# Kernel tuning notes

Measured on AMD Instinct MI355X. Metric: run time of the kernel, lower is better.

## Reference

```python
import jax, jax.numpy as jnp
import numpy as np

EMBED_DIM = 768
HIDDEN = 768


def setup_inputs() -> dict:
    key = jax.random.key(0)
    k1, k2, k3, k4 = jax.random.split(key, 4)
    doc_embed = jax.random.normal(k1, (32, 1024, EMBED_DIM), dtype=jnp.float32)
    query_embed = jax.random.normal(k2, (32, 128, EMBED_DIM), dtype=jnp.float32)
    # nn.Linear params: weight [H, E], bias [H]
    bound = 1.0 / np.sqrt(EMBED_DIM)
    W = jax.random.uniform(k3, (HIDDEN, EMBED_DIM), minval=-bound, maxval=bound, dtype=jnp.float32)
    b = jax.random.uniform(k4, (HIDDEN,), minval=-bound, maxval=bound, dtype=jnp.float32)
    return {"doc_embed": doc_embed, "query_embed": query_embed, "W": W, "b": b}


def reference(doc_embed, query_embed, W, b):
    # shared linear projection + ReLU
    doc_o = jax.nn.relu(jnp.einsum('bde,he->bdh', doc_embed, W) + b)    # [B, Ld, H]
    query_o = jax.nn.relu(jnp.einsum('bqe,he->bqh', query_embed, W) + b)  # [B, Lq, H]
    # unscaled cross-attention scores over query positions
    scores = jnp.einsum('bdh,bqh->bdq', doc_o, query_o)  # [B, Ld, Lq]
    attn = jax.nn.softmax(scores, axis=-1)
    out = jnp.einsum('bdq,bqe->bde', attn, query_embed)  # [B, Ld, E]
    return out
```

## Files before the change

### kernel.cpp

```cpp
#include <hip/hip_runtime.h>

typedef _Float16 f16x8 __attribute__((ext_vector_type(8)));
typedef float f32x4 __attribute__((ext_vector_type(4)));

#define EMB 768
#define LQ 128
#define LD 1024
#define NB 32

typedef const __attribute__((address_space(1))) char gas_char;
typedef __attribute__((address_space(3))) char las_char;

__device__ __forceinline__ void gload16(const void* g, void* l) {
    __builtin_amdgcn_global_load_lds((gas_char*)g, (las_char*)l, 16, 0, 0);
}

#define SWZ(row, ch) ((row) * 64 + ((((ch) ^ ((row) & 7))) * 8))

__device__ __forceinline__ void stage_tile(const _Float16* g, _Float16* l, int wave, int lane) {
#pragma unroll
    for (int i = 0; i < 4; ++i) {
        const int idx = i * 256 + wave * 64 + lane;
        const int row = idx >> 3, ch = idx & 7;
        const int lch = ch ^ (row & 7);
        gload16(g + (size_t)row * EMB + lch * 8, l + (size_t)(i * 256 + wave * 64) * 8);
    }
}

__global__ void cvt8_kernel(const float* __restrict__ in, _Float16* __restrict__ out, int n8) {
    int i = blockIdx.x * 256 + threadIdx.x;
    if (i >= n8) return;
    const float4 a = ((const float4*)in)[2 * i];
    const float4 b = ((const float4*)in)[2 * i + 1];
    f16x8 o;
    o[0] = (_Float16)a.x; o[1] = (_Float16)a.y; o[2] = (_Float16)a.z; o[3] = (_Float16)a.w;
    o[4] = (_Float16)b.x; o[5] = (_Float16)b.y; o[6] = (_Float16)b.z; o[7] = (_Float16)b.w;
    ((f16x8*)out)[i] = o;
}

__global__ void make_vt_kernel(const float* __restrict__ Q, _Float16* __restrict__ VT) {
    int i = blockIdx.x * 256 + threadIdx.x;
    if (i >= NB * EMB * LQ) return;
    int q = i % LQ;
    int e = (i / LQ) % EMB;
    int b = i / (LQ * EMB);
    VT[i] = (_Float16)Q[((size_t)b * LQ + q) * EMB + e];
}

__global__ __launch_bounds__(256) void proj128_kernel(
    const _Float16* __restrict__ A, const _Float16* __restrict__ B,
    const float* __restrict__ bias, _Float16* __restrict__ OUT) {
    __shared__ __align__(16) _Float16 smem[32768];
    const int tid = threadIdx.x, wave = tid >> 6, lane = tid & 63;
    const int wr = wave >> 1, wc = wave & 1;
    const int lr = lane & 15, lkg = lane >> 4;
    const int row0 = blockIdx.x * 128, col0 = blockIdx.y * 128;
    const _Float16* ga = A + (size_t)row0 * EMB;
    const _Float16* gb = B + (size_t)col0 * EMB;

    f32x4 acc[4][4];
#pragma unroll
    for (int m = 0; m < 4; ++m)
#pragma unroll
        for (int n = 0; n < 4; ++n) acc[m][n] = (f32x4){0.f, 0.f, 0.f, 0.f};

    stage_tile(ga, smem, wave, lane);
    stage_tile(gb, smem + 8192, wave, lane);
    int cur = 0;
    for (int it = 0; it < 12; ++it) {
        __syncthreads();
        if (it < 11) {
            stage_tile(ga + (it + 1) * 64, smem + (cur ^ 1) * 16384, wave, lane);
            stage_tile(gb + (it + 1) * 64, smem + (cur ^ 1) * 16384 + 8192, wave, lane);
        }
        const _Float16* sA = smem + cur * 16384;
        const _Float16* sB = smem + cur * 16384 + 8192;
#pragma unroll
        for (int kk = 0; kk < 2; ++kk) {
            const int ch = kk * 4 + lkg;
            f16x8 af[4], bf[4];
#pragma unroll
            for (int m = 0; m < 4; ++m)
                af[m] = *(const f16x8*)(sA + SWZ(wr * 64 + m * 16 + lr, ch));
#pragma unroll
            for (int n = 0; n < 4; ++n)
                bf[n] = *(const f16x8*)(sB + SWZ(wc * 64 + n * 16 + lr, ch));
#pragma unroll
            for (int m = 0; m < 4; ++m)
#pragma unroll
                for (int n = 0; n < 4; ++n)
                    acc[m][n] = __builtin_amdgcn_mfma_f32_16x16x32_f16(af[m], bf[n], acc[m][n], 0, 0, 0);
        }
        cur ^= 1;
    }
    const int crow = lkg * 4;
#pragma unroll
    for (int n = 0; n < 4; ++n) {
        const int gc = col0 + wc * 64 + n * 16 + lr;
        const float bv = bias[gc];
#pragma unroll
        for (int m = 0; m < 4; ++m) {
            const size_t gr = row0 + wr * 64 + m * 16 + crow;
#pragma unroll
            for (int r = 0; r < 4; ++r) {
                float v = acc[m][n][r] + bv;
                OUT[(gr + r) * EMB + gc] = (_Float16)(v > 0.f ? v : 0.f);
            }
        }
    }
}

__global__ __launch_bounds__(256) void attn128_kernel(
    const _Float16* __restrict__ Do, const _Float16* __restrict__ Qo,
    const _Float16* __restrict__ VT, float* __restrict__ OUT) {
    __shared__ __align__(16) _Float16 smem[32768];
    const int tid = threadIdx.x, wave = tid >> 6, lane = tid & 63;
    const int lr = lane & 15, lkg = lane >> 4;
    const int b = blockIdx.x, dblk = blockIdx.y;
    const _Float16* gd = Do + ((size_t)b * LD + dblk * 128) * EMB;
    const _Float16* gq = Qo + (size_t)b * LQ * EMB;

    f32x4 s[2][8];
#pragma unroll
    for (int m = 0; m < 2; ++m)
#pragma unroll
        for (int n = 0; n < 8; ++n) s[m][n] = (f32x4){0.f, 0.f, 0.f, 0.f};

    stage_tile(gd, smem, wave, lane);
    stage_tile(gq, smem + 8192, wave, lane);
    int cur = 0;
    for (int it = 0; it < 12; ++it) {
        __syncthreads();
        if (it < 11) {
            stage_tile(gd + (it + 1) * 64, smem + (cur ^ 1) * 16384, wave, lane);
            stage_tile(gq + (it + 1) * 64, smem + (cur ^ 1) * 16384 + 8192, wave, lane);
        }
        const _Float16* sD = smem + cur * 16384;
        const _Float16* sQ = smem + cur * 16384 + 8192;
#pragma unroll
        for (int kk = 0; kk < 2; ++kk) {
            const int ch = kk * 4 + lkg;
            f16x8 am[2];
#pragma unroll
            for (int m = 0; m < 2; ++m)
                am[m] = *(const f16x8*)(sD + SWZ(wave * 32 + m * 16 + lr, ch));
#pragma unroll
            for (int n = 0; n < 8; ++n) {
                const f16x8 bq = *(const f16x8*)(sQ + SWZ(n * 16 + lr, ch));
#pragma unroll
                for (int m = 0; m < 2; ++m)
                    s[m][n] = __builtin_amdgcn_mfma_f32_16x16x32_f16(am[m], bq, s[m][n], 0, 0, 0);
            }
        }
        cur ^= 1;
    }
    __syncthreads();

    _Float16 (*P)[136] = (_Float16 (*)[136])smem;
    const int crow = lkg * 4;
#pragma unroll
    for (int m = 0; m < 2; ++m) {
#pragma unroll
        for (int r = 0; r < 4; ++r) {
            float mx = -1e30f;
#pragma unroll
            for (int n = 0; n < 8; ++n) mx = fmaxf(mx, s[m][n][r]);
#pragma unroll
            for (int off = 1; off < 16; off <<= 1) mx = fmaxf(mx, __shfl_xor(mx, off));
            float p[8], sum = 0.f;
#pragma unroll
            for (int n = 0; n < 8; ++n) { p[n] = __expf(s[m][n][r] - mx); sum += p[n]; }
#pragma unroll
            for (int off = 1; off < 16; off <<= 1) sum += __shfl_xor(sum, off);
            const float inv = 1.f / sum;
            const int row = wave * 32 + m * 16 + crow + r;
#pragma unroll
            for (int n = 0; n < 8; ++n) P[row][n * 16 + lr] = (_Float16)(p[n] * inv);
        }
    }
    __syncthreads();

    const _Float16* vtb = VT + (size_t)b * EMB * LQ;
#pragma unroll 1
    for (int nc = 0; nc < 6; ++nc) {
        f32x4 o[2][8];
#pragma unroll
        for (int m = 0; m < 2; ++m)
#pragma unroll
            for (int t = 0; t < 8; ++t) o[m][t] = (f32x4){0.f, 0.f, 0.f, 0.f};
#pragma unroll
        for (int ks = 0; ks < 4; ++ks) {
            f16x8 am[2];
#pragma unroll
            for (int m = 0; m < 2; ++m)
                am[m] = *(const f16x8*)(&P[wave * 32 + m * 16 + lr][ks * 32 + lkg * 8]);
#pragma unroll
            for (int t = 0; t < 8; ++t) {
                const f16x8 bv = *(const f16x8*)(vtb + (size_t)(nc * 128 + t * 16 + lr) * LQ + ks * 32 + lkg * 8);
#pragma unroll
                for (int m = 0; m < 2; ++m)
                    o[m][t] = __builtin_amdgcn_mfma_f32_16x16x32_f16(am[m], bv, o[m][t], 0, 0, 0);
            }
        }
#pragma unroll
        for (int t = 0; t < 8; ++t) {
#pragma unroll
            for (int m = 0; m < 2; ++m) {
                const size_t gr = (size_t)b * LD + dblk * 128 + wave * 32 + m * 16 + crow;
                const int e = nc * 128 + t * 16 + lr;
#pragma unroll
                for (int r = 0; r < 4; ++r)
                    OUT[(gr + r) * EMB + e] = o[m][t][r];
            }
        }
    }
}

extern "C" void kernel_launch(void* const* d_in, const int* in_sizes, int n_in,
                              void* d_out, int out_size, void* d_ws, size_t ws_size,
                              hipStream_t stream) {
    const float* doc   = (const float*)d_in[0];
    const float* query = (const float*)d_in[1];
    const float* W     = (const float*)d_in[2];
    const float* bias  = (const float*)d_in[3];
    float* out = (float*)d_out;

    const size_t nW  = (size_t)EMB * EMB;
    const size_t nVT = (size_t)NB * EMB * LQ;
    const size_t nQo = (size_t)NB * LQ * EMB;
    const size_t nDo = (size_t)NB * LD * EMB;
    const size_t need = (nW + nVT + nQo + nDo) * sizeof(_Float16);
    if (ws_size < need) return;

    _Float16* W16 = (_Float16*)d_ws;
    _Float16* VT  = W16 + nW;
    _Float16* Qo  = VT + nVT;
    _Float16* Do  = Qo + nQo;

    _Float16* doc16 = (_Float16*)d_out;
    _Float16* q16   = doc16 + nDo;

    cvt8_kernel<<<(int)(nDo / 8 / 256), 256, 0, stream>>>(doc, doc16, (int)(nDo / 8));
    cvt8_kernel<<<(int)(nQo / 8 / 256), 256, 0, stream>>>(query, q16, (int)(nQo / 8));
    cvt8_kernel<<<(int)(nW / 8 / 256), 256, 0, stream>>>(W, W16, (int)(nW / 8));
    make_vt_kernel<<<(int)(nVT / 256), 256, 0, stream>>>(query, VT);

    proj128_kernel<<<dim3(NB * LQ / 128, EMB / 128), 256, 0, stream>>>(q16, W16, bias, Qo);
    proj128_kernel<<<dim3(NB * LD / 128, EMB / 128), 256, 0, stream>>>(doc16, W16, bias, Do);
    attn128_kernel<<<dim3(NB, LD / 128), 256, 0, stream>>>(Do, Qo, VT, out);
}
```

Baseline: 160.1 us.

## Replace projection GEMM with 256x256 ping-pong scheduled kernel fusing doc and query

Replaces the 128x128 projection kernel with a 512-thread kernel that computes 256x256 output tiles, using 128KB of dynamic LDS with double buffering. It interleaves global-to-LDS staging with MFMA quarter-steps through explicit barriers, waitcnts and setprio, and remaps the grid so neighbouring blocks share tiles. The workspace is reordered so the doc and query outputs are contiguous, matching the contiguous fp16 inputs, and both projections run in a single launch. The goals are more data reuse per tile, better overlap of loads with MFMA work, and one fewer launch. The cost is a fragile hand-written schedule, only one block per CU, and a hipFuncSetAttribute call on every launch.

```diff
diff --git a/kernel.cpp b/kernel.cpp
--- a/kernel.cpp
+++ b/kernel.cpp
@@ -17,15 +17,10 @@
 
 #define SWZ(row, ch) ((row) * 64 + ((((ch) ^ ((row) & 7))) * 8))
 
-__device__ __forceinline__ void stage_tile(const _Float16* g, _Float16* l, int wave, int lane) {
-#pragma unroll
-    for (int i = 0; i < 4; ++i) {
-        const int idx = i * 256 + wave * 64 + lane;
-        const int row = idx >> 3, ch = idx & 7;
-        const int lch = ch ^ (row & 7);
-        gload16(g + (size_t)row * EMB + lch * 8, l + (size_t)(i * 256 + wave * 64) * 8);
-    }
-}
+#define BAR() asm volatile("s_barrier" ::: "memory")
+#define LGKM0() do { asm volatile("s_waitcnt lgkmcnt(0)" ::: "memory"); \
+                     __builtin_amdgcn_sched_barrier(0); } while (0)
+#define VMW(N) asm volatile("s_waitcnt vmcnt(" #N ")" ::: "memory")
 
 __global__ void cvt8_kernel(const float* __restrict__ in, _Float16* __restrict__ out, int n8) {
     int i = blockIdx.x * 256 + threadIdx.x;
@@ -47,60 +42,104 @@
     VT[i] = (_Float16)Q[((size_t)b * LQ + q) * EMB + e];
 }
 
-__global__ __launch_bounds__(256) void proj128_kernel(
-    const _Float16* __restrict__ A, const _Float16* __restrict__ B,
+__device__ __forceinline__ void stage_tile(const _Float16* g, _Float16* l, int tid) {
+#pragma unroll
+    for (int i = 0; i < 4; ++i) {
+        const int idx = i * 256 + tid;
+        const int row = idx >> 3, ch = idx & 7;
+        gload16(g + (size_t)row * EMB + ((ch ^ (row & 7)) * 8), l + (size_t)idx * 8);
+    }
+}
+
+__global__ __launch_bounds__(512, 2) void proj8_kernel(
+    const _Float16* __restrict__ A, const _Float16* __restrict__ W16,
     const float* __restrict__ bias, _Float16* __restrict__ OUT) {
-    __shared__ __align__(16) _Float16 smem[32768];
+    extern __shared__ _Float16 smem[];
     const int tid = threadIdx.x, wave = tid >> 6, lane = tid & 63;
-    const int wr = wave >> 1, wc = wave & 1;
     const int lr = lane & 15, lkg = lane >> 4;
-    const int row0 = blockIdx.x * 128, col0 = blockIdx.y * 128;
-    const _Float16* ga = A + (size_t)row0 * EMB;
-    const _Float16* gb = B + (size_t)col0 * EMB;
-
-    f32x4 acc[4][4];
-#pragma unroll
-    for (int m = 0; m < 4; ++m)
+    const int wr = wave >> 2, wc = wave & 3;
+
+    const int nwg = gridDim.x, cpx = nwg >> 3;
+    const int swz = (blockIdx.x & 7) * cpx + (blockIdx.x >> 3);
+    const int rowblk = swz / 3, colblk = swz - rowblk * 3;
+    const int row0 = rowblk * 256, col0 = colblk * 256;
+
+    const int r0_ = tid >> 3, c0_ = (((tid & 7) ^ (r0_ & 7)) * 8);
+    const int r1_ = (512 + tid) >> 3, c1_ = ((((512 + tid) & 7) ^ (r1_ & 7)) * 8);
+    const int lo0 = tid * 8, lo1 = (512 + tid) * 8;
+
+    const _Float16* gA0 = A + (size_t)row0 * EMB;
+    const _Float16* gA1 = A + (size_t)(row0 + 128) * EMB;
+    const _Float16* gB0 = W16 + (size_t)col0 * EMB;
+    const _Float16* gB1 = W16 + (size_t)(col0 + 128) * EMB;
+
+#define STAGE_PAIR(g0, g1, kt, lbase) do { \
+    const _Float16* s0_ = (g0) + (kt) * 64; const _Float16* s1_ = (g1) + (kt) * 64; \
+    _Float16* d_ = (lbase); \
+    gload16(s0_ + (size_t)r0_ * EMB + c0_, d_ + lo0); \
+    gload16(s0_ + (size_t)r1_ * EMB + c1_, d_ + lo1); \
+    gload16(s1_ + (size_t)r0_ * EMB + c0_, d_ + 8192 + lo0); \
+    gload16(s1_ + (size_t)r1_ * EMB + c1_, d_ + 8192 + lo1); } while (0)
+
+    f32x4 acc[8][4];
+#pragma unroll
+    for (int m = 0; m < 8; ++m)
 #pragma unroll
         for (int n = 0; n < 4; ++n) acc[m][n] = (f32x4){0.f, 0.f, 0.f, 0.f};
 
-    stage_tile(ga, smem, wave, lane);
-    stage_tile(gb, smem + 8192, wave, lane);
-    int cur = 0;
-    for (int it = 0; it < 12; ++it) {
-        __syncthreads();
-        if (it < 11) {
-            stage_tile(ga + (it + 1) * 64, smem + (cur ^ 1) * 16384, wave, lane);
-            stage_tile(gb + (it + 1) * 64, smem + (cur ^ 1) * 16384 + 8192, wave, lane);
-        }
-        const _Float16* sA = smem + cur * 16384;
-        const _Float16* sB = smem + cur * 16384 + 8192;
-#pragma unroll
-        for (int kk = 0; kk < 2; ++kk) {
-            const int ch = kk * 4 + lkg;
-            f16x8 af[4], bf[4];
-#pragma unroll
-            for (int m = 0; m < 4; ++m)
-                af[m] = *(const f16x8*)(sA + SWZ(wr * 64 + m * 16 + lr, ch));
-#pragma unroll
-            for (int n = 0; n < 4; ++n)
-                bf[n] = *(const f16x8*)(sB + SWZ(wc * 64 + n * 16 + lr, ch));
-#pragma unroll
-            for (int m = 0; m < 4; ++m)
-#pragma unroll
-                for (int n = 0; n < 4; ++n)
-                    acc[m][n] = __builtin_amdgcn_mfma_f32_16x16x32_f16(af[m], bf[n], acc[m][n], 0, 0, 0);
-        }
-        cur ^= 1;
-    }
+    f16x8 aF[4][2], bF[4][2];
+    const int bro = (wc & 1) * 64;
+
+#define READ_A(slot, MH) do { _Float16* ab_ = smem + (slot) * 32768 + wr * 8192; \
+    _Pragma("unroll") for (int mm = 0; mm < 4; ++mm) _Pragma("unroll") for (int ks = 0; ks < 2; ++ks) \
+        aF[mm][ks] = *(const f16x8*)(ab_ + SWZ(((MH) * 4 + mm) * 16 + lr, ks * 4 + lkg)); } while (0)
+#define READ_B(slot, NH) do { _Float16* bb_ = smem + (slot) * 32768 + 16384 + (wc >> 1) * 8192; \
+    _Pragma("unroll") for (int nn = 0; nn < 2; ++nn) _Pragma("unroll") for (int ks = 0; ks < 2; ++ks) \
+        bF[(NH) * 2 + nn][ks] = *(const f16x8*)(bb_ + SWZ(bro + ((NH) * 2 + nn) * 16 + lr, ks * 4 + lkg)); } while (0)
+#define MFMA_Q(MH, NH) do { __builtin_amdgcn_s_setprio(1); \
+    _Pragma("unroll") for (int mm = 0; mm < 4; ++mm) _Pragma("unroll") for (int nn = 0; nn < 2; ++nn) \
+    _Pragma("unroll") for (int ks = 0; ks < 2; ++ks) \
+        acc[(MH) * 4 + mm][(NH) * 2 + nn] = __builtin_amdgcn_mfma_f32_16x16x32_f16( \
+            aF[mm][ks], bF[(NH) * 2 + nn][ks], acc[(MH) * 4 + mm][(NH) * 2 + nn], 0, 0, 0); \
+    __builtin_amdgcn_s_setprio(0); } while (0)
+
+    STAGE_PAIR(gB0, gB1, 0, smem + 16384);
+    STAGE_PAIR(gA0, gA1, 0, smem);
+    STAGE_PAIR(gB0, gB1, 1, smem + 32768 + 16384);
+    STAGE_PAIR(gA0, gA1, 1, smem + 32768);
+    VMW(8);
+    BAR();
+
+#pragma unroll 1
+    for (int j = 0; j < 6; ++j) {
+        const int kt2 = 2 * j + 2, kt3 = 2 * j + 3;
+        READ_B(0, 0); READ_B(0, 1); READ_A(0, 0);
+        BAR(); LGKM0(); MFMA_Q(0, 0); BAR();
+        BAR(); LGKM0(); MFMA_Q(0, 1); BAR();
+        READ_A(0, 1);
+        if (j < 5) STAGE_PAIR(gB0, gB1, kt2, smem + 16384);
+        BAR(); LGKM0(); MFMA_Q(1, 0); BAR();
+        if (j < 5) { STAGE_PAIR(gA0, gA1, kt2, smem); VMW(4); }
+        else       { VMW(0); }
+        BAR(); LGKM0(); MFMA_Q(1, 1); BAR();
+        READ_B(1, 0); READ_B(1, 1); READ_A(1, 0);
+        BAR(); LGKM0(); MFMA_Q(0, 0); BAR();
+        BAR(); LGKM0(); MFMA_Q(0, 1); BAR();
+        READ_A(1, 1);
+        if (j < 5) STAGE_PAIR(gB0, gB1, kt3, smem + 32768 + 16384);
+        BAR(); LGKM0(); MFMA_Q(1, 0); BAR();
+        if (j < 5) { STAGE_PAIR(gA0, gA1, kt3, smem + 32768); VMW(4); }
+        BAR(); LGKM0(); MFMA_Q(1, 1); BAR();
+    }
+
     const int crow = lkg * 4;
 #pragma unroll
     for (int n = 0; n < 4; ++n) {
         const int gc = col0 + wc * 64 + n * 16 + lr;
         const float bv = bias[gc];
 #pragma unroll
-        for (int m = 0; m < 4; ++m) {
-            const size_t gr = row0 + wr * 64 + m * 16 + crow;
+        for (int m = 0; m < 8; ++m) {
+            const size_t gr = (size_t)row0 + wr * 128 + m * 16 + crow;
 #pragma unroll
             for (int r = 0; r < 4; ++r) {
                 float v = acc[m][n][r] + bv;
@@ -108,6 +147,10 @@
             }
         }
     }
+#undef STAGE_PAIR
+#undef READ_A
+#undef READ_B
+#undef MFMA_Q
 }
 
 __global__ __launch_bounds__(256) void attn128_kernel(
@@ -126,17 +169,17 @@
 #pragma unroll
         for (int n = 0; n < 8; ++n) s[m][n] = (f32x4){0.f, 0.f, 0.f, 0.f};
 
-    stage_tile(gd, smem, wave, lane);
-    stage_tile(gq, smem + 8192, wave, lane);
+    stage_tile(gd, smem, tid);
+    stage_tile(gq, smem + 8192, tid);
     int cur = 0;
     for (int it = 0; it < 12; ++it) {
         __syncthreads();
         if (it < 11) {
-            stage_tile(gd + (it + 1) * 64, smem + (cur ^ 1) * 16384, wave, lane);
-            stage_tile(gq + (it + 1) * 64, smem + (cur ^ 1) * 16384 + 8192, wave, lane);
+            stage_tile(gd + (it + 1) * 64, smem + (cur ^ 1) * 16384, tid);
+            stage_tile(gq + (it + 1) * 64, smem + (cur ^ 1) * 16384 + 8192, tid);
         }
         const _Float16* sD = smem + cur * 16384;
-        const _Float16* sQ = smem + cur * 16384 + 8192;
+        const _Float16* sQ = sD + 8192;
 #pragma unroll
         for (int kk = 0; kk < 2; ++kk) {
             const int ch = kk * 4 + lkg;
@@ -227,15 +270,15 @@
 
     const size_t nW  = (size_t)EMB * EMB;
     const size_t nVT = (size_t)NB * EMB * LQ;
+    const size_t nDo = (size_t)NB * LD * EMB;
     const size_t nQo = (size_t)NB * LQ * EMB;
-    const size_t nDo = (size_t)NB * LD * EMB;
-    const size_t need = (nW + nVT + nQo + nDo) * sizeof(_Float16);
+    const size_t need = (nW + nVT + nDo + nQo) * sizeof(_Float16);
     if (ws_size < need) return;
 
     _Float16* W16 = (_Float16*)d_ws;
     _Float16* VT  = W16 + nW;
-    _Float16* Qo  = VT + nVT;
-    _Float16* Do  = Qo + nQo;
+    _Float16* Do  = VT + nVT;
+    _Float16* Qo  = Do + nDo;
 
     _Float16* doc16 = (_Float16*)d_out;
     _Float16* q16   = doc16 + nDo;
@@ -245,7 +288,9 @@
     cvt8_kernel<<<(int)(nW / 8 / 256), 256, 0, stream>>>(W, W16, (int)(nW / 8));
     make_vt_kernel<<<(int)(nVT / 256), 256, 0, stream>>>(query, VT);
 
-    proj128_kernel<<<dim3(NB * LQ / 128, EMB / 128), 256, 0, stream>>>(q16, W16, bias, Qo);
-    proj128_kernel<<<dim3(NB * LD / 128, EMB / 128), 256, 0, stream>>>(doc16, W16, bias, Do);
+    hipFuncSetAttribute(reinterpret_cast<const void*>(&proj8_kernel),
+                        hipFuncAttributeMaxDynamicSharedMemorySize, 131072);
+    proj8_kernel<<<dim3(144 * 3), 512, 131072, stream>>>(doc16, W16, bias, Do);
+
     attn128_kernel<<<dim3(NB, LD / 128), 256, 0, stream>>>(Do, Qo, VT, out);
 }
```

After: 154.6 us. 1.04x faster.
